# Performance work log

Measured on AMD Instinct MI355X. Metric: run time of the kernel, lower is better.

Reference implementation:

```python
import jax, jax.numpy as jnp
import numpy as np

B, T, H, O = 256, 2048, 64, 2


def setup_inputs() -> dict:
    key = jax.random.key(0)
    ks = jax.random.split(key, 14)
    def lin(k, out_f, in_f):
        bound = np.sqrt(6.0 / (in_f + out_f))
        return jax.random.uniform(k, (out_f, in_f), jnp.float32, -bound, bound)
    return {
        "x": jax.random.normal(ks[0], (B, T, 2), jnp.float32),
        "h0": jax.random.normal(ks[1], (1, B, H), jnp.float32),
        "Wa": lin(ks[2], H, H + 1), "ba": jnp.zeros((H,), jnp.float32),
        "Wp1": lin(ks[3], H, H + 1), "bp1": jnp.zeros((H,), jnp.float32),
        "Wp2": lin(ks[4], H, H + 1), "bp2": jnp.zeros((H,), jnp.float32),
        "Wf": lin(ks[5], H, 2 * H), "bf": jnp.zeros((H,), jnp.float32),
        "Wg": lin(ks[6], H, 2 * H), "bg": jnp.zeros((H,), jnp.float32),
        "Wo": lin(ks[7], O, H), "bo": jnp.zeros((O,), jnp.float32),
    }


def reference(x, h0, Wa, ba, Wp1, bp1, Wp2, bp2, Wf, bf, Wg, bg, Wo, bo):
    # x: [B, T, 2] (I/Q), h0: [1, B, H]
    xt = jnp.swapaxes(x, 0, 1)  # [T, B, 2]

    def step(h, x_t):
        i = x_t[:, 0:1]
        q = x_t[:, 1:2]
        amp = jnp.sqrt(i * i + q * q)
        theta = jnp.arctan2(q, i)
        cos_t = jnp.cos(theta)
        sin_t = jnp.sin(theta)
        a = jnp.tanh(jnp.concatenate([h, amp], -1) @ Wa.T + ba)
        p1 = jnp.tanh(jnp.concatenate([h, cos_t], -1) @ Wp1.T + bp1)
        p2 = jnp.tanh(jnp.concatenate([h, sin_t], -1) @ Wp2.T + bp2)
        u = a * p1 * p2 * (1 - a) * (1 - p1) * (1 - p2)
        hu = jnp.concatenate([h, u], -1)
        f = jax.nn.sigmoid(hu @ Wf.T + bf)
        g = jnp.tanh(hu @ Wg.T + bg)
        h_new = f * h + (1 - f) * g
        y = h_new @ Wo.T + bo
        return h_new, y

    _, ys = jax.lax.scan(step, h0[0], xt)  # ys: [T, B, O]
    return jnp.swapaxes(ys, 0, 1)  # [B, T, O]
```

## Files before the change

### kernel.cpp

```cpp
#include <hip/hip_runtime.h>
#include <math.h>

#define BB 256
#define TT 2048
#define HH 64

typedef _Float16 half2v __attribute__((ext_vector_type(2)));
typedef __fp16  fp16v2 __attribute__((ext_vector_type(2)));
union H2I { half2v h; int i; };

#if __has_builtin(__builtin_amdgcn_rcpf)
__device__ __forceinline__ float fast_rcp(float v) { return __builtin_amdgcn_rcpf(v); }
#else
__device__ __forceinline__ float fast_rcp(float v) { return 1.0f / v; }
#endif
#if __has_builtin(__builtin_amdgcn_rsqf)
__device__ __forceinline__ float fast_rsq(float v) { return __builtin_amdgcn_rsqf(v); }
#else
__device__ __forceinline__ float fast_rsq(float v) { return rsqrtf(v); }
#endif

__device__ __forceinline__ float tanh_fast(float v) {
    float e = __expf(2.0f * v);
    return fmaf(-2.0f, fast_rcp(e + 1.0f), 1.0f);
}

__device__ __forceinline__ float sigmoid_fast(float v) {
    return fast_rcp(1.0f + __expf(-v));
}

__device__ __forceinline__ float fdot2(half2v a, half2v b, float c) {
    return __builtin_amdgcn_fdot2(a, b, c, false);
}

__device__ __forceinline__ half2v pack_pair(float a, float b) {
    fp16v2 r = __builtin_amdgcn_cvt_pkrtz(a, b);
    return __builtin_bit_cast(half2v, r);
}

__device__ __forceinline__ void pin_h2(half2v& v) {
    H2I u; u.h = v;
    asm volatile("" : "+v"(u.i));
    v = u.h;
}

__device__ __forceinline__ half2v bcast_pair(half2v v, int lane) {
    H2I u; u.h = v;
    H2I w; w.i = __builtin_amdgcn_readlane(u.i, lane);
    return w.h;
}

__device__ __forceinline__ float dpp_neighbor(float v) {
    return __int_as_float(__builtin_amdgcn_mov_dpp(__float_as_int(v), 0xB1, 0xf, 0xf, true));
}

__global__ __launch_bounds__(64, 1)
void pgjanet_kernel(const float* __restrict__ x,
                    const float* __restrict__ h0,
                    const float* __restrict__ Wa,  const float* __restrict__ ba,
                    const float* __restrict__ Wp1, const float* __restrict__ bp1,
                    const float* __restrict__ Wp2, const float* __restrict__ bp2,
                    const float* __restrict__ Wf,  const float* __restrict__ bf,
                    const float* __restrict__ Wg,  const float* __restrict__ bg,
                    const float* __restrict__ Wo,  const float* __restrict__ bo,
                    float* __restrict__ out)
{
    const int b = blockIdx.x;
    const int j = threadIdx.x;

    __shared__ float xs[TT * 2];
    __shared__ float hbuf[64][HH + 1];
    __shared__ float woLDS[2 * HH];

    {
        const float4* xp4 = reinterpret_cast<const float4*>(x + (size_t)b * (TT * 2));
        float4*       xs4 = reinterpret_cast<float4*>(xs);
#pragma unroll
        for (int i = 0; i < (TT * 2 / 4) / 64; ++i) xs4[j + 64 * i] = xp4[j + 64 * i];
    }
    for (int i = j; i < 2 * HH; i += 64) woLDS[i] = Wo[i];

    half2v w5[5][32], wfu[32], wgu[32];
    {
        const float* Wsrc[5] = {Wa, Wp1, Wp2, Wf, Wg};
        const int    ldv[5]  = {HH + 1, HH + 1, HH + 1, 2 * HH, 2 * HH};
#pragma unroll
        for (int g = 0; g < 5; ++g) {
            const float* r = Wsrc[g] + (size_t)j * ldv[g];
#pragma unroll
            for (int m = 0; m < 32; ++m) w5[g][m] = pack_pair(r[2 * m], r[2 * m + 1]);
        }
        const float* rf = Wf + (size_t)j * (2 * HH) + HH;
        const float* rg = Wg + (size_t)j * (2 * HH) + HH;
#pragma unroll
        for (int m = 0; m < 32; ++m) {
            wfu[m] = pack_pair(rf[2 * m], rf[2 * m + 1]);
            wgu[m] = pack_pair(rg[2 * m], rg[2 * m + 1]);
        }
#pragma unroll
        for (int g = 0; g < 5; ++g)
#pragma unroll
            for (int m = 0; m < 32; ++m) pin_h2(w5[g][m]);
#pragma unroll
        for (int m = 0; m < 32; ++m) { pin_h2(wfu[m]); pin_h2(wgu[m]); }
    }

    const float waX  = Wa [j * (HH + 1) + HH];
    const float wp1X = Wp1[j * (HH + 1) + HH];
    const float wp2X = Wp2[j * (HH + 1) + HH];
    const float ba_r = ba[j], bp1_r = bp1[j], bp2_r = bp2[j];
    const float bf_r = bf[j], bg_r = bg[j];
    const float bo0  = bo[0], bo1 = bo[1];

    float  h  = h0[b * HH + j];
    float* yp = out + (size_t)b * (TT * 2);

    __syncthreads();

    float amp, ct, st;
    {
        float xi = xs[0], xq = xs[1];
        float r2 = xi * xi + xq * xq;
        float rq = fast_rsq(r2);
        bool ok = r2 > 0.f;
        amp = ok ? r2 * rq : 0.f;
        ct  = ok ? xi * rq : 1.f;
        st  = ok ? xq * rq : 0.f;
    }

    for (int t = 0; t < TT; ++t) {
        const int tn = (t + 1 < TT) ? (t + 1) : t;
        float xi_n = xs[2 * tn], xq_n = xs[2 * tn + 1];
        float amp_n, ct_n, st_n;
        {
            float r2 = xi_n * xi_n + xq_n * xq_n;
            float rq = fast_rsq(r2);
            bool ok = r2 > 0.f;
            amp_n = ok ? r2 * rq : 0.f;
            ct_n  = ok ? xi_n * rq : 1.f;
            st_n  = ok ? xq_n * rq : 0.f;
        }

        float  hnbr = dpp_neighbor(h);
        half2v hp   = pack_pair(h, hnbr);
        half2v sh[32];
#pragma unroll
        for (int m = 0; m < 32; ++m) sh[m] = bcast_pair(hp, 2 * m);

        float acc[5];
        acc[0] = fmaf(amp, waX,  ba_r);
        acc[1] = fmaf(ct,  wp1X, bp1_r);
        acc[2] = fmaf(st,  wp2X, bp2_r);
        acc[3] = bf_r;
        acc[4] = bg_r;
#pragma unroll
        for (int m = 0; m < 32; ++m)
#pragma unroll
            for (int g = 0; g < 5; ++g)
                acc[g] = fdot2(sh[m], w5[g][m], acc[g]);

        float av = tanh_fast(acc[0]);
        float p1 = tanh_fast(acc[1]);
        float p2 = tanh_fast(acc[2]);
        float u = fmaf(-av, av, av) * fmaf(-p1, p1, p1) * fmaf(-p2, p2, p2);

        float  unbr = dpp_neighbor(u);
        half2v up   = pack_pair(u, unbr);
        half2v su[32];
#pragma unroll
        for (int m = 0; m < 32; ++m) su[m] = bcast_pair(up, 2 * m);

        float f0 = acc[3], f1 = 0.f, g0 = acc[4], g1 = 0.f;
#pragma unroll
        for (int m = 0; m < 16; ++m) {
            f0 = fdot2(su[m],      wfu[m],      f0);
            f1 = fdot2(su[m + 16], wfu[m + 16], f1);
            g0 = fdot2(su[m],      wgu[m],      g0);
            g1 = fdot2(su[m + 16], wgu[m + 16], g1);
        }
        float f = sigmoid_fast(f0 + f1);
        float g = tanh_fast(g0 + g1);
        h = fmaf(f, h - g, g);

        hbuf[t & 63][j] = h;

        if ((t & 63) == 63) {
            float y0 = bo0, y1 = bo1;
#pragma unroll 4
            for (int k = 0; k < HH; ++k) {
                float hv = hbuf[j][k];
                y0 = fmaf(hv, woLDS[k],      y0);
                y1 = fmaf(hv, woLDS[HH + k], y1);
            }
            reinterpret_cast<float2*>(yp)[(t - 63) + j] = make_float2(y0, y1);
        }

        amp = amp_n; ct = ct_n; st = st_n;
    }
}

extern "C" void kernel_launch(void* const* d_in, const int* in_sizes, int n_in,
                              void* d_out, int out_size, void* d_ws, size_t ws_size,
                              hipStream_t stream) {
    const float* x   = (const float*)d_in[0];
    const float* h0  = (const float*)d_in[1];
    const float* Wa  = (const float*)d_in[2];
    const float* ba  = (const float*)d_in[3];
    const float* Wp1 = (const float*)d_in[4];
    const float* bp1 = (const float*)d_in[5];
    const float* Wp2 = (const float*)d_in[6];
    const float* bp2 = (const float*)d_in[7];
    const float* Wf  = (const float*)d_in[8];
    const float* bf  = (const float*)d_in[9];
    const float* Wg  = (const float*)d_in[10];
    const float* bg  = (const float*)d_in[11];
    const float* Wo  = (const float*)d_in[12];
    const float* bo  = (const float*)d_in[13];
    float* out = (float*)d_out;

    pgjanet_kernel<<<dim3(BB), dim3(64), 0, stream>>>(
        x, h0, Wa, ba, Wp1, bp1, Wp2, bp2, Wf, bf, Wg, bg, Wo, bo, out);
}
```

Baseline: 1.478 ms.

## Split recurrent gate matvec across two waves with per-step LDS exchange

Each block now runs two waves. Each wave computes half of the K-dimension of the five hidden-state gate dot products, and the partial sums are exchanged through double-buffered LDS with a block barrier every timestep. Both waves then redundantly finish the u, f and g stages and the state update. The amplitude, cos and sin input features are precomputed for all timesteps into LDS up front. The output projection is split so each wave produces one output channel. The goal is to halve the serial dot-product chain per step, at the cost of a barrier and an LDS round trip on the critical path of every step.

```diff
diff --git a/kernel.cpp b/kernel.cpp
--- a/kernel.cpp
+++ b/kernel.cpp
@@ -54,7 +54,7 @@
     return __int_as_float(__builtin_amdgcn_mov_dpp(__float_as_int(v), 0xB1, 0xf, 0xf, true));
 }
 
-__global__ __launch_bounds__(64, 1)
+__global__ __launch_bounds__(128, 1)
 void pgjanet_kernel(const float* __restrict__ x,
                     const float* __restrict__ h0,
                     const float* __restrict__ Wa,  const float* __restrict__ ba,
@@ -65,30 +65,38 @@
                     const float* __restrict__ Wo,  const float* __restrict__ bo,
                     float* __restrict__ out)
 {
-    const int b = blockIdx.x;
-    const int j = threadIdx.x;
-
-    __shared__ float xs[TT * 2];
-    __shared__ float hbuf[64][HH + 1];
-    __shared__ float woLDS[2 * HH];
-
-    {
-        const float4* xp4 = reinterpret_cast<const float4*>(x + (size_t)b * (TT * 2));
-        float4*       xs4 = reinterpret_cast<float4*>(xs);
-#pragma unroll
-        for (int i = 0; i < (TT * 2 / 4) / 64; ++i) xs4[j + 64 * i] = xp4[j + 64 * i];
+    const int b   = blockIdx.x;
+    const int tid = threadIdx.x;
+    const int j   = tid & 63;
+    const int w   = __builtin_amdgcn_readfirstlane(tid >> 6);
+
+    __shared__ float4 xt[TT];
+    __shared__ float  hbuf[64][HH + 1];
+    __shared__ float  woLDS[2 * HH];
+    __shared__ float2 exAB[2][2][2][64];
+    __shared__ float  exC [2][2][64];
+
+    for (int t = tid; t < TT; t += 128) {
+        float2 xi = reinterpret_cast<const float2*>(x)[(size_t)b * TT + t];
+        float r2 = xi.x * xi.x + xi.y * xi.y;
+        float rq = fast_rsq(r2);
+        bool ok = r2 > 0.f;
+        xt[t] = make_float4(ok ? r2 * rq : 0.f,
+                            ok ? xi.x * rq : 1.f,
+                            ok ? xi.y * rq : 0.f,
+                            0.f);
     }
-    for (int i = j; i < 2 * HH; i += 64) woLDS[i] = Wo[i];
-
-    half2v w5[5][32], wfu[32], wgu[32];
+    for (int i = tid; i < 2 * HH; i += 128) woLDS[i] = Wo[i];
+
+    half2v w5h[5][16], wfu[32], wgu[32];
     {
         const float* Wsrc[5] = {Wa, Wp1, Wp2, Wf, Wg};
         const int    ldv[5]  = {HH + 1, HH + 1, HH + 1, 2 * HH, 2 * HH};
 #pragma unroll
         for (int g = 0; g < 5; ++g) {
-            const float* r = Wsrc[g] + (size_t)j * ldv[g];
-#pragma unroll
-            for (int m = 0; m < 32; ++m) w5[g][m] = pack_pair(r[2 * m], r[2 * m + 1]);
+            const float* r = Wsrc[g] + (size_t)j * ldv[g] + 32 * w;
+#pragma unroll
+            for (int m = 0; m < 16; ++m) w5h[g][m] = pack_pair(r[2 * m], r[2 * m + 1]);
         }
         const float* rf = Wf + (size_t)j * (2 * HH) + HH;
         const float* rg = Wg + (size_t)j * (2 * HH) + HH;
@@ -100,7 +108,7 @@
 #pragma unroll
         for (int g = 0; g < 5; ++g)
 #pragma unroll
-            for (int m = 0; m < 32; ++m) pin_h2(w5[g][m]);
+            for (int m = 0; m < 16; ++m) pin_h2(w5h[g][m]);
 #pragma unroll
         for (int m = 0; m < 32; ++m) { pin_h2(wfu[m]); pin_h2(wgu[m]); }
     }
@@ -110,73 +118,61 @@
     const float wp2X = Wp2[j * (HH + 1) + HH];
     const float ba_r = ba[j], bp1_r = bp1[j], bp2_r = bp2[j];
     const float bf_r = bf[j], bg_r = bg[j];
-    const float bo0  = bo[0], bo1 = bo[1];
-
-    float  h  = h0[b * HH + j];
-    float* yp = out + (size_t)b * (TT * 2);
+    const float bo_w = (w == 0) ? bo[0] : bo[1];
+
+    float h = h0[b * HH + j];
 
     __syncthreads();
 
-    float amp, ct, st;
-    {
-        float xi = xs[0], xq = xs[1];
-        float r2 = xi * xi + xq * xq;
-        float rq = fast_rsq(r2);
-        bool ok = r2 > 0.f;
-        amp = ok ? r2 * rq : 0.f;
-        ct  = ok ? xi * rq : 1.f;
-        st  = ok ? xq * rq : 0.f;
-    }
-
     for (int t = 0; t < TT; ++t) {
-        const int tn = (t + 1 < TT) ? (t + 1) : t;
-        float xi_n = xs[2 * tn], xq_n = xs[2 * tn + 1];
-        float amp_n, ct_n, st_n;
-        {
-            float r2 = xi_n * xi_n + xq_n * xq_n;
-            float rq = fast_rsq(r2);
-            bool ok = r2 > 0.f;
-            amp_n = ok ? r2 * rq : 0.f;
-            ct_n  = ok ? xi_n * rq : 1.f;
-            st_n  = ok ? xq_n * rq : 0.f;
-        }
+        const int par = t & 1;
+        float4 xv = xt[t];
 
         float  hnbr = dpp_neighbor(h);
         half2v hp   = pack_pair(h, hnbr);
-        half2v sh[32];
-#pragma unroll
-        for (int m = 0; m < 32; ++m) sh[m] = bcast_pair(hp, 2 * m);
-
-        float acc[5];
-        acc[0] = fmaf(amp, waX,  ba_r);
-        acc[1] = fmaf(ct,  wp1X, bp1_r);
-        acc[2] = fmaf(st,  wp2X, bp2_r);
-        acc[3] = bf_r;
-        acc[4] = bg_r;
-#pragma unroll
-        for (int m = 0; m < 32; ++m)
-#pragma unroll
-            for (int g = 0; g < 5; ++g)
-                acc[g] = fdot2(sh[m], w5[g][m], acc[g]);
-
-        float av = tanh_fast(acc[0]);
-        float p1 = tanh_fast(acc[1]);
-        float p2 = tanh_fast(acc[2]);
-        float u = fmaf(-av, av, av) * fmaf(-p1, p1, p1) * fmaf(-p2, p2, p2);
+
+        float p0 = 0.f, p1v = 0.f, p2v = 0.f, p3 = 0.f, p4 = 0.f;
+#pragma unroll
+        for (int m = 0; m < 16; ++m) {
+            half2v s = bcast_pair(hp, 32 * w + 2 * m);
+            p0  = fdot2(s, w5h[0][m], p0);
+            p1v = fdot2(s, w5h[1][m], p1v);
+            p2v = fdot2(s, w5h[2][m], p2v);
+            p3  = fdot2(s, w5h[3][m], p3);
+            p4  = fdot2(s, w5h[4][m], p4);
+        }
+
+        exAB[par][w][0][j] = make_float2(p0, p1v);
+        exAB[par][w][1][j] = make_float2(p2v, p3);
+        exC [par][w][j]    = p4;
+        __syncthreads();
+        float2 o01 = exAB[par][w ^ 1][0][j];
+        float2 o23 = exAB[par][w ^ 1][1][j];
+        float  oc  = exC [par][w ^ 1][j];
+
+        float acc0 = (p0  + o01.x) + fmaf(xv.x, waX,  ba_r);
+        float acc1 = (p1v + o01.y) + fmaf(xv.y, wp1X, bp1_r);
+        float acc2 = (p2v + o23.x) + fmaf(xv.z, wp2X, bp2_r);
+        float acc3 = (p3  + o23.y) + bf_r;
+        float acc4 = (p4  + oc)    + bg_r;
+
+        float av = tanh_fast(acc0);
+        float q1 = tanh_fast(acc1);
+        float q2 = tanh_fast(acc2);
+        float u = fmaf(-av, av, av) * fmaf(-q1, q1, q1) * fmaf(-q2, q2, q2);
 
         float  unbr = dpp_neighbor(u);
         half2v up   = pack_pair(u, unbr);
-        half2v su[32];
-#pragma unroll
-        for (int m = 0; m < 32; ++m) su[m] = bcast_pair(up, 2 * m);
-
-        float f0 = acc[3], f1 = 0.f, g0 = acc[4], g1 = 0.f;
+
+        float f0 = acc3, f1 = 0.f, g0 = acc4, g1 = 0.f;
 #pragma unroll
         for (int m = 0; m < 16; ++m) {
-            f0 = fdot2(su[m],      wfu[m],      f0);
-            f1 = fdot2(su[m + 16], wfu[m + 16], f1);
-            g0 = fdot2(su[m],      wgu[m],      g0);
-            g1 = fdot2(su[m + 16], wgu[m + 16], g1);
+            half2v s0 = bcast_pair(up, 2 * m);
+            half2v s1 = bcast_pair(up, 2 * (m + 16));
+            f0 = fdot2(s0, wfu[m],      f0);
+            f1 = fdot2(s1, wfu[m + 16], f1);
+            g0 = fdot2(s0, wgu[m],      g0);
+            g1 = fdot2(s1, wgu[m + 16], g1);
         }
         float f = sigmoid_fast(f0 + f1);
         float g = tanh_fast(g0 + g1);
@@ -185,17 +181,13 @@
         hbuf[t & 63][j] = h;
 
         if ((t & 63) == 63) {
-            float y0 = bo0, y1 = bo1;
+            const float* worow = &woLDS[w * HH];
+            float y = bo_w;
 #pragma unroll 4
-            for (int k = 0; k < HH; ++k) {
-                float hv = hbuf[j][k];
-                y0 = fmaf(hv, woLDS[k],      y0);
-                y1 = fmaf(hv, woLDS[HH + k], y1);
-            }
-            reinterpret_cast<float2*>(yp)[(t - 63) + j] = make_float2(y0, y1);
-        }
-
-        amp = amp_n; ct = ct_n; st = st_n;
+            for (int k = 0; k < HH; ++k)
+                y = fmaf(hbuf[j][k], worow[k], y);
+            out[(size_t)b * (TT * 2) + 2 * ((t - 63) + j) + w] = y;
+        }
     }
 }
 
@@ -218,6 +210,6 @@
     const float* bo  = (const float*)d_in[13];
     float* out = (float*)d_out;
 
-    pgjanet_kernel<<<dim3(BB), dim3(64), 0, stream>>>(
+    pgjanet_kernel<<<dim3(BB), dim3(128), 0, stream>>>(
         x, h0, Wa, ba, Wp1, bp1, Wp2, bp2, Wf, bf, Wg, bg, Wo, bo, out);
 }
```

Measured after the change: 1.586 ms. +7.3%, slower.

## Broadcast packed hidden state through LDS instead of readlane, precompute polar inputs

Applied to the files above, without the earlier changes.

Each step, the even lanes write their packed fp16 pairs of h (and later u) to a small LDS buffer. The whole wave then reads that buffer back as eight 128-bit loads, replacing 32 v_readlane broadcasts per vector. Separately, amp/cos/sin for all timesteps are computed once in the prologue and stored as float4 in LDS, so the per-step rsqrt math leaves the loop. This trades readlane SGPR traffic for two LDS write/read round trips per step on the serial recurrence, relying on a single wavefront for ordering without barriers.

```diff
diff --git a/kernel.cpp b/kernel.cpp
--- a/kernel.cpp
+++ b/kernel.cpp
@@ -7,7 +7,7 @@
 
 typedef _Float16 half2v __attribute__((ext_vector_type(2)));
 typedef __fp16  fp16v2 __attribute__((ext_vector_type(2)));
-union H2I { half2v h; int i; };
+union H2I { half2v h; unsigned int i; };
 
 #if __has_builtin(__builtin_amdgcn_rcpf)
 __device__ __forceinline__ float fast_rcp(float v) { return __builtin_amdgcn_rcpf(v); }
@@ -44,14 +44,13 @@
     v = u.h;
 }
 
-__device__ __forceinline__ half2v bcast_pair(half2v v, int lane) {
-    H2I u; u.h = v;
-    H2I w; w.i = __builtin_amdgcn_readlane(u.i, lane);
-    return w.h;
-}
-
 __device__ __forceinline__ float dpp_neighbor(float v) {
     return __int_as_float(__builtin_amdgcn_mov_dpp(__float_as_int(v), 0xB1, 0xf, 0xf, true));
+}
+
+__device__ __forceinline__ half2v h2_from_u32(unsigned int w) {
+    H2I u; u.i = w;
+    return u.h;
 }
 
 __global__ __launch_bounds__(64, 1)
@@ -68,15 +67,21 @@
     const int b = blockIdx.x;
     const int j = threadIdx.x;
 
-    __shared__ float xs[TT * 2];
-    __shared__ float hbuf[64][HH + 1];
-    __shared__ float woLDS[2 * HH];
-
-    {
-        const float4* xp4 = reinterpret_cast<const float4*>(x + (size_t)b * (TT * 2));
-        float4*       xs4 = reinterpret_cast<float4*>(xs);
-#pragma unroll
-        for (int i = 0; i < (TT * 2 / 4) / 64; ++i) xs4[j + 64 * i] = xp4[j + 64 * i];
+    __shared__ float4 xt[TT];
+    __shared__ float  hbuf[64][HH + 1];
+    __shared__ float  woLDS[2 * HH];
+    __shared__ __align__(16) unsigned int hpk[32];
+    __shared__ __align__(16) unsigned int upk[32];
+
+    for (int t = j; t < TT; t += 64) {
+        float2 xi = reinterpret_cast<const float2*>(x)[(size_t)b * TT + t];
+        float r2 = xi.x * xi.x + xi.y * xi.y;
+        float rq = fast_rsq(r2);
+        bool ok = r2 > 0.f;
+        xt[t] = make_float4(ok ? r2 * rq : 0.f,
+                            ok ? xi.x * rq : 1.f,
+                            ok ? xi.y * rq : 0.f,
+                            0.f);
     }
     for (int i = j; i < 2 * HH; i += 64) woLDS[i] = Wo[i];
 
@@ -117,66 +122,68 @@
 
     __syncthreads();
 
-    float amp, ct, st;
-    {
-        float xi = xs[0], xq = xs[1];
-        float r2 = xi * xi + xq * xq;
-        float rq = fast_rsq(r2);
-        bool ok = r2 > 0.f;
-        amp = ok ? r2 * rq : 0.f;
-        ct  = ok ? xi * rq : 1.f;
-        st  = ok ? xq * rq : 0.f;
-    }
+    float4 xv = xt[0];
 
     for (int t = 0; t < TT; ++t) {
         const int tn = (t + 1 < TT) ? (t + 1) : t;
-        float xi_n = xs[2 * tn], xq_n = xs[2 * tn + 1];
-        float amp_n, ct_n, st_n;
+        float4 xv_n = xt[tn];
+
         {
-            float r2 = xi_n * xi_n + xq_n * xq_n;
-            float rq = fast_rsq(r2);
-            bool ok = r2 > 0.f;
-            amp_n = ok ? r2 * rq : 0.f;
-            ct_n  = ok ? xi_n * rq : 1.f;
-            st_n  = ok ? xq_n * rq : 0.f;
-        }
-
-        float  hnbr = dpp_neighbor(h);
-        half2v hp   = pack_pair(h, hnbr);
-        half2v sh[32];
-#pragma unroll
-        for (int m = 0; m < 32; ++m) sh[m] = bcast_pair(hp, 2 * m);
-
-        float acc[5];
-        acc[0] = fmaf(amp, waX,  ba_r);
-        acc[1] = fmaf(ct,  wp1X, bp1_r);
-        acc[2] = fmaf(st,  wp2X, bp2_r);
-        acc[3] = bf_r;
-        acc[4] = bg_r;
-#pragma unroll
-        for (int m = 0; m < 32; ++m)
-#pragma unroll
-            for (int g = 0; g < 5; ++g)
-                acc[g] = fdot2(sh[m], w5[g][m], acc[g]);
-
-        float av = tanh_fast(acc[0]);
-        float p1 = tanh_fast(acc[1]);
-        float p2 = tanh_fast(acc[2]);
+            float hn = dpp_neighbor(h);
+            H2I hp; hp.h = pack_pair(h, hn);
+            if ((j & 1) == 0) hpk[j >> 1] = hp.i;
+        }
+        uint4 hw[8];
+#pragma unroll
+        for (int i = 0; i < 8; ++i) hw[i] = reinterpret_cast<const uint4*>(hpk)[i];
+
+        float acc0 = fmaf(xv.x, waX,  ba_r);
+        float acc1 = fmaf(xv.y, wp1X, bp1_r);
+        float acc2 = fmaf(xv.z, wp2X, bp2_r);
+        float acc3 = bf_r;
+        float acc4 = bg_r;
+#pragma unroll
+        for (int i = 0; i < 8; ++i) {
+#pragma unroll
+            for (int q = 0; q < 4; ++q) {
+                const int m = 4 * i + q;
+                half2v s = h2_from_u32((&hw[i].x)[q]);
+                acc0 = fdot2(s, w5[0][m], acc0);
+                acc1 = fdot2(s, w5[1][m], acc1);
+                acc2 = fdot2(s, w5[2][m], acc2);
+                acc3 = fdot2(s, w5[3][m], acc3);
+                acc4 = fdot2(s, w5[4][m], acc4);
+            }
+        }
+
+        float av = tanh_fast(acc0);
+        float p1 = tanh_fast(acc1);
+        float p2 = tanh_fast(acc2);
         float u = fmaf(-av, av, av) * fmaf(-p1, p1, p1) * fmaf(-p2, p2, p2);
 
-        float  unbr = dpp_neighbor(u);
-        half2v up   = pack_pair(u, unbr);
-        half2v su[32];
-#pragma unroll
-        for (int m = 0; m < 32; ++m) su[m] = bcast_pair(up, 2 * m);
-
-        float f0 = acc[3], f1 = 0.f, g0 = acc[4], g1 = 0.f;
-#pragma unroll
-        for (int m = 0; m < 16; ++m) {
-            f0 = fdot2(su[m],      wfu[m],      f0);
-            f1 = fdot2(su[m + 16], wfu[m + 16], f1);
-            g0 = fdot2(su[m],      wgu[m],      g0);
-            g1 = fdot2(su[m + 16], wgu[m + 16], g1);
+        {
+            float un = dpp_neighbor(u);
+            H2I up; up.h = pack_pair(u, un);
+            if ((j & 1) == 0) upk[j >> 1] = up.i;
+        }
+        uint4 uw[8];
+#pragma unroll
+        for (int i = 0; i < 8; ++i) uw[i] = reinterpret_cast<const uint4*>(upk)[i];
+
+        float f0 = acc3, f1 = 0.f, g0 = acc4, g1 = 0.f;
+#pragma unroll
+        for (int i = 0; i < 4; ++i) {
+#pragma unroll
+            for (int q = 0; q < 4; ++q) {
+                const int m  = 4 * i + q;
+                const int m2 = m + 16;
+                half2v s0 = h2_from_u32((&uw[i].x)[q]);
+                half2v s1 = h2_from_u32((&uw[i + 4].x)[q]);
+                f0 = fdot2(s0, wfu[m],  f0);
+                f1 = fdot2(s1, wfu[m2], f1);
+                g0 = fdot2(s0, wgu[m],  g0);
+                g1 = fdot2(s1, wgu[m2], g1);
+            }
         }
         float f = sigmoid_fast(f0 + f1);
         float g = tanh_fast(g0 + g1);
@@ -195,7 +202,7 @@
             reinterpret_cast<float2*>(yp)[(t - 63) + j] = make_float2(y0, y1);
         }
 
-        amp = amp_n; ct = ct_n; st = st_n;
+        xv = xv_n;
     }
 }
 
```

Result: slower. 1.514 ms (+2.4%).
